# Kernel optimization log

Hardware: AMD Instinct MI355X
Metric: run time of the kernel (lower is better)

Reference implementation:

```python
import jax, jax.numpy as jnp
import numpy as np
from jax import lax

B, L = 1, 2048
D_MODEL = 768
D_INNER = 1536          # expand(2) * d_model
D_STATE = 16
DT_RANK = 48            # ceil(768/16)
D_CONV = 4
N_LAYER = 4
VOCAB = 50264           # 50257 padded to multiple of 8
EPS = 1e-5


def setup_inputs() -> dict:
    key = jax.random.key(0)
    ks = jax.random.split(key, 10)
    sc = 0.02
    input_ids = jax.random.randint(ks[0], (B, L), 0, VOCAB)
    emb = jax.random.normal(ks[1], (VOCAB, D_MODEL), jnp.float32) * sc
    in_proj_w = jax.random.normal(ks[2], (N_LAYER, 2 * D_INNER, D_MODEL), jnp.float32) * sc
    conv_w = jax.random.normal(ks[3], (N_LAYER, D_INNER, D_CONV), jnp.float32) * 0.1
    conv_b = jnp.zeros((N_LAYER, D_INNER), jnp.float32)
    x_proj_w = jax.random.normal(ks[4], (N_LAYER, DT_RANK + 2 * D_STATE, D_INNER), jnp.float32) * sc
    dt_proj_w = jax.random.normal(ks[5], (N_LAYER, D_INNER, DT_RANK), jnp.float32) * 0.1
    dt_proj_b = jax.random.normal(ks[6], (N_LAYER, D_INNER), jnp.float32) * 0.1
    # A_log initialized as log(1..d_state) repeated over d_inner (as in module init)
    A_row = jnp.log(jnp.arange(1, D_STATE + 1, dtype=jnp.float32))
    A_log = jnp.broadcast_to(A_row, (N_LAYER, D_INNER, D_STATE)).copy()
    D_param = jnp.ones((N_LAYER, D_INNER), jnp.float32)
    out_proj_w = jax.random.normal(ks[7], (N_LAYER, D_MODEL, D_INNER), jnp.float32) * sc
    norm_w = jnp.ones((N_LAYER, D_MODEL), jnp.float32)
    norm_f_w = jnp.ones((D_MODEL,), jnp.float32)
    return {
        'input_ids': input_ids, 'emb': emb, 'in_proj_w': in_proj_w,
        'conv_w': conv_w, 'conv_b': conv_b, 'x_proj_w': x_proj_w,
        'dt_proj_w': dt_proj_w, 'dt_proj_b': dt_proj_b, 'A_log': A_log,
        'D_param': D_param, 'out_proj_w': out_proj_w, 'norm_w': norm_w,
        'norm_f_w': norm_f_w,
    }


def _rmsnorm(x, w):
    return x * lax.rsqrt(jnp.mean(x * x, axis=-1, keepdims=True) + EPS) * w


def _selective_scan(u, delta, A, Bm, Cm, Dv):
    # u, delta: (b,l,d_in); A: (d_in,n); Bm, Cm: (b,l,n); Dv: (d_in,)
    deltaA = jnp.exp(delta[..., None] * A)                       # (b,l,d_in,n)
    deltaB_u = delta[..., None] * Bm[:, :, None, :] * u[..., None]  # (b,l,d_in,n)
    b = u.shape[0]
    h0 = jnp.zeros((b, D_INNER, D_STATE), u.dtype)

    def step(h, inp):
        dA_t, dBu_t, C_t = inp
        h = dA_t * h + dBu_t                                     # (b,d_in,n)
        y = jnp.einsum('bdn,bn->bd', h, C_t)
        return h, y

    xs = (jnp.swapaxes(deltaA, 0, 1), jnp.swapaxes(deltaB_u, 0, 1),
          jnp.swapaxes(Cm, 0, 1))
    _, ys = lax.scan(step, h0, xs)                               # (l,b,d_in)
    y = jnp.swapaxes(ys, 0, 1)
    return y + u * Dv


def _mamba_block(x, in_w, cw, cb, xp_w, dtp_w, dtp_b, A_log, Dv, out_w):
    b, l, _ = x.shape
    x_and_res = x @ in_w.T                                       # (b,l,2*d_in)
    xi, res = x_and_res[..., :D_INNER], x_and_res[..., D_INNER:]
    # depthwise causal conv1d
    xc = jnp.swapaxes(xi, 1, 2)                                  # (b,d_in,l)
    xc = lax.conv_general_dilated(
        xc, cw[:, None, :], window_strides=(1,), padding=[(D_CONV - 1, 0)],
        feature_group_count=D_INNER, dimension_numbers=('NCH', 'OIH', 'NCH'))
    xc = xc + cb[None, :, None]
    xi = jax.nn.silu(jnp.swapaxes(xc, 1, 2))                     # (b,l,d_in)
    # ssm
    A = -jnp.exp(A_log)
    x_dbl = xi @ xp_w.T                                          # (b,l,dt_rank+2n)
    delta = x_dbl[..., :DT_RANK]
    Bm = x_dbl[..., DT_RANK:DT_RANK + D_STATE]
    Cm = x_dbl[..., DT_RANK + D_STATE:]
    delta = jax.nn.softplus(delta @ dtp_w.T + dtp_b)             # (b,l,d_in)
    y = _selective_scan(xi, delta, A, Bm, Cm, Dv)
    y = y * jax.nn.silu(res)
    return y @ out_w.T


def reference(input_ids, emb, in_proj_w, conv_w, conv_b, x_proj_w,
              dt_proj_w, dt_proj_b, A_log, D_param, out_proj_w,
              norm_w, norm_f_w):
    x = emb[input_ids]                                           # (b,l,d_model)
    for i in range(N_LAYER):
        h = _rmsnorm(x, norm_w[i])
        x = x + _mamba_block(h, in_proj_w[i], conv_w[i], conv_b[i],
                             x_proj_w[i], dt_proj_w[i], dt_proj_b[i],
                             A_log[i], D_param[i], out_proj_w[i])
    x = _rmsnorm(x, norm_f_w)
    logits = x @ emb.T                                           # tied lm_head
    return logits
```

## Files before the change

### kernel.cpp

```cpp
#include <hip/hip_runtime.h>
#include <hip/hip_bf16.h>
#include <math.h>

#define LSEQ 2048
#define DMODEL 768
#define DINNER 1536
#define DSTATE 16
#define DTRANK 48
#define NLAYER 4
#define XDBL_W 80
#define CH 64
#define SLEN 32

typedef __attribute__((ext_vector_type(4))) float f32x4;
typedef __attribute__((ext_vector_type(8))) short short8;
typedef __attribute__((ext_vector_type(8))) __bf16 bf16x8;
typedef __attribute__((ext_vector_type(4))) unsigned short us4;

__device__ inline float softplus_f(float x) {
    return fmaxf(x, 0.f) + log1pf(expf(-fabsf(x)));
}
__device__ inline float silu_f(float x) {
    return x / (1.f + expf(-x));
}

__device__ inline unsigned short f2bf(float f) {
    unsigned int u = __float_as_uint(f);
    unsigned int r = (u + 0x7fffu + ((u >> 16) & 1u)) >> 16;
    return (unsigned short)r;
}
__device__ inline float bf2f(unsigned short b) {
    return __uint_as_float((unsigned int)b << 16);
}

__device__ inline f32x4 mfma_bf16_16x16x32(short8 a, short8 b, f32x4 c) {
    return __builtin_amdgcn_mfma_f32_16x16x32_bf16(
        __builtin_bit_cast(bf16x8, a), __builtin_bit_cast(bf16x8, b), c, 0, 0, 0);
}

#define GLDS16(gp, lp) __builtin_amdgcn_global_load_lds( \
    (const __attribute__((address_space(1))) void*)(gp), \
    (__attribute__((address_space(3))) void*)(lp), 16, 0, 0)

__global__ __launch_bounds__(256) void embed_kernel(
    const int* __restrict__ ids, const float* __restrict__ emb,
    float* __restrict__ x)
{
    int l = blockIdx.x;
    int id = ids[l];
    const float* src = emb + (size_t)id * DMODEL;
    float* dst = x + (size_t)l * DMODEL;
    for (int j = threadIdx.x; j < DMODEL; j += 256) dst[j] = src[j];
}

__global__ __launch_bounds__(256) void rmsnorm_kernel(
    const float* __restrict__ x, const float* __restrict__ w,
    float* __restrict__ o)
{
    int row = blockIdx.x;
    const float* xr = x + (size_t)row * DMODEL;
    float ss = 0.f;
    for (int j = threadIdx.x; j < DMODEL; j += 256) { float v = xr[j]; ss += v * v; }
    __shared__ float red[256];
    red[threadIdx.x] = ss;
    __syncthreads();
    for (int s = 128; s > 0; s >>= 1) {
        if (threadIdx.x < s) red[threadIdx.x] += red[threadIdx.x + s];
        __syncthreads();
    }
    float scale = rsqrtf(red[0] / DMODEL + 1e-5f);
    for (int j = threadIdx.x; j < DMODEL; j += 256)
        o[(size_t)row * DMODEL + j] = xr[j] * scale * w[j];
}

#define BM 64
#define BN 64
#define BK 16
__global__ __launch_bounds__(256) void gemm_nt(
    const float* __restrict__ A, const float* __restrict__ B,
    float* __restrict__ C, int M, int N, int K,
    int lda, int ldb, int ldc, int mode, const float* __restrict__ bias)
{
    __shared__ float As[BK][BM + 4];
    __shared__ float Bs[BK][BN + 4];
    int tid = threadIdx.x;
    int tx = tid & 15;
    int ty = tid >> 4;
    int row0 = blockIdx.y * BM;
    int col0 = blockIdx.x * BN;

    int lm = tid >> 2;
    int lk = (tid & 3) * 4;

    float acc[4][4];
#pragma unroll
    for (int i = 0; i < 4; ++i)
#pragma unroll
        for (int j = 0; j < 4; ++j) acc[i][j] = 0.f;

    for (int k0 = 0; k0 < K; k0 += BK) {
        {
            int gm = row0 + lm;
            float4 v = make_float4(0.f, 0.f, 0.f, 0.f);
            if (gm < M) v = *(const float4*)(A + (size_t)gm * lda + k0 + lk);
            As[lk + 0][lm] = v.x; As[lk + 1][lm] = v.y;
            As[lk + 2][lm] = v.z; As[lk + 3][lm] = v.w;
            int gn = col0 + lm;
            float4 w = make_float4(0.f, 0.f, 0.f, 0.f);
            if (gn < N) w = *(const float4*)(B + (size_t)gn * ldb + k0 + lk);
            Bs[lk + 0][lm] = w.x; Bs[lk + 1][lm] = w.y;
            Bs[lk + 2][lm] = w.z; Bs[lk + 3][lm] = w.w;
        }
        __syncthreads();
#pragma unroll
        for (int k = 0; k < BK; ++k) {
            float4 a = *(const float4*)(&As[k][ty * 4]);
            float4 b = *(const float4*)(&Bs[k][tx * 4]);
            float av[4] = { a.x, a.y, a.z, a.w };
            float bv[4] = { b.x, b.y, b.z, b.w };
#pragma unroll
            for (int i = 0; i < 4; ++i)
#pragma unroll
                for (int j = 0; j < 4; ++j) acc[i][j] += av[i] * bv[j];
        }
        __syncthreads();
    }

#pragma unroll
    for (int i = 0; i < 4; ++i) {
        int m = row0 + ty * 4 + i;
        if (m >= M) continue;
#pragma unroll
        for (int j = 0; j < 4; ++j) {
            int n = col0 + tx * 4 + j;
            if (n >= N) continue;
            float v = acc[i][j];
            if (mode == 1) v = softplus_f(v + bias[n]);
            else if (mode == 2) v += C[(size_t)m * ldc + n];
            C[(size_t)m * ldc + n] = v;
        }
    }
}

__global__ __launch_bounds__(256) void split_bf16_kernel(
    const float* __restrict__ src, unsigned short* __restrict__ hi,
    unsigned short* __restrict__ lo, long long srcElems, long long totElems)
{
    long long idx = ((long long)blockIdx.x * 256 + threadIdx.x) * 4;
    if (idx >= totElems) return;
    float4 v = make_float4(0.f, 0.f, 0.f, 0.f);
    if (idx < srcElems) v = *(const float4*)(src + idx);
    unsigned short h0 = f2bf(v.x), h1 = f2bf(v.y), h2 = f2bf(v.z), h3 = f2bf(v.w);
    us4 hv = { h0, h1, h2, h3 };
    us4 lv = { f2bf(v.x - bf2f(h0)), f2bf(v.y - bf2f(h1)),
               f2bf(v.z - bf2f(h2)), f2bf(v.w - bf2f(h3)) };
    *(us4*)(hi + idx) = hv;
    *(us4*)(lo + idx) = lv;
}

__global__ __launch_bounds__(256) void gemm_logits_mfma(
    const unsigned short* __restrict__ Ah, const unsigned short* __restrict__ Al,
    const unsigned short* __restrict__ Bh, const unsigned short* __restrict__ Bl,
    float* __restrict__ C, int N)
{
    __shared__ unsigned short As[128 * 32];
    __shared__ unsigned short Bs[128 * 32];
    int tid = threadIdx.x;
    int lane = tid & 63;
    int wid = tid >> 6;
    int wrow = wid >> 1, wcol = wid & 1;
    int brow0 = blockIdx.x * 128;
    int bcol0 = blockIdx.y * 128;

    f32x4 acc[4][4];
#pragma unroll
    for (int m = 0; m < 4; ++m)
#pragma unroll
        for (int n = 0; n < 4; ++n) acc[m][n] = (f32x4){ 0.f, 0.f, 0.f, 0.f };

    int arow = brow0 + wid * 32 + (lane >> 2);
    int bcol = bcol0 + wid * 32 + (lane >> 2);
    int kb = (lane & 3) * 8;
    char* lbaseA = (char*)As + wid * 2048;
    char* lbaseB = (char*)Bs + wid * 2048;

    for (int vb = 0; vb < 3; ++vb) {
        const unsigned short* Ab = (vb == 1) ? Al : Ah;
        const unsigned short* Bb = (vb == 2) ? Bl : Bh;
        for (int k0 = 0; k0 < DMODEL; k0 += 32) {
#pragma unroll
            for (int j = 0; j < 2; ++j) {
                GLDS16(Ab + (size_t)(arow + j * 16) * DMODEL + k0 + kb, lbaseA + j * 1024);
                GLDS16(Bb + (size_t)(bcol + j * 16) * DMODEL + k0 + kb, lbaseB + j * 1024);
            }
            __syncthreads();
            short8 af[4], bfr[4];
#pragma unroll
            for (int m = 0; m < 4; ++m)
                af[m] = *(const short8*)(As + ((wrow * 64 + m * 16 + (lane & 15)) * 32 + (lane >> 4) * 8));
#pragma unroll
            for (int n = 0; n < 4; ++n)
                bfr[n] = *(const short8*)(Bs + ((wcol * 64 + n * 16 + (lane & 15)) * 32 + (lane >> 4) * 8));
#pragma unroll
            for (int m = 0; m < 4; ++m)
#pragma unroll
                for (int n = 0; n < 4; ++n)
                    acc[m][n] = mfma_bf16_16x16x32(af[m], bfr[n], acc[m][n]);
            __syncthreads();
        }
    }

    int r0 = brow0 + wrow * 64 + (lane >> 4) * 4;
    int c0 = bcol0 + wcol * 64 + (lane & 15);
#pragma unroll
    for (int m = 0; m < 4; ++m)
#pragma unroll
        for (int n = 0; n < 4; ++n) {
            int col = c0 + n * 16;
            if (col >= N) continue;
#pragma unroll
            for (int i = 0; i < 4; ++i)
                C[(size_t)(r0 + m * 16 + i) * N + col] = acc[m][n][i];
        }
}

__global__ __launch_bounds__(256) void conv_silu_kernel(
    const float* __restrict__ xr, const float* __restrict__ cw,
    const float* __restrict__ cb, float* __restrict__ u)
{
    int idx = blockIdx.x * 256 + threadIdx.x;
    if (idx >= LSEQ * DINNER) return;
    int l = idx / DINNER;
    int d = idx - l * DINNER;
    float s = cb[d];
#pragma unroll
    for (int t = 0; t < 4; ++t) {
        int ll = l - 3 + t;
        if (ll >= 0) s += xr[(size_t)ll * (2 * DINNER) + d] * cw[d * 4 + t];
    }
    u[idx] = silu_f(s);
}

__global__ __launch_bounds__(256) void neg_exp_kernel(
    const float* __restrict__ a, float* __restrict__ o, int n)
{
    int i = blockIdx.x * 256 + threadIdx.x;
    if (i < n) o[i] = -expf(a[i]);
}

__global__ __launch_bounds__(256) void scan_phase1(
    const float* __restrict__ delta, const float* __restrict__ u,
    const float* __restrict__ xdbl, const float* __restrict__ Aneg,
    float* __restrict__ cA, float* __restrict__ cB)
{
    int tid = threadIdx.x;
    int n = tid & 15;
    int d = blockIdx.x * 16 + (tid >> 4);
    int c = blockIdx.y;
    float Av = Aneg[d * DSTATE + n];
    float h = 0.f, ap = 1.f;
    int l = c * SLEN;
    for (int s = 0; s < SLEN; ++s, ++l) {
        float dt = delta[(size_t)l * DINNER + d];
        float uv = u[(size_t)l * DINNER + d];
        float Bv = xdbl[l * XDBL_W + DTRANK + n];
        float a = expf(dt * Av);
        h = a * h + dt * Bv * uv;
        ap *= a;
    }
    size_t off = ((size_t)c * DINNER + d) * DSTATE + n;
    cA[off] = ap;
    cB[off] = h;
}

__global__ __launch_bounds__(256) void scan_phase2(
    const float* __restrict__ cA, const float* __restrict__ cB,
    float* __restrict__ hs)
{
    int idx = blockIdx.x * 256 + threadIdx.x;
    float h = 0.f;
    for (int c = 0; c < CH; ++c) {
        size_t off = (size_t)c * DINNER * DSTATE + idx;
        hs[off] = h;
        h = cA[off] * h + cB[off];
    }
}

__global__ __launch_bounds__(256) void scan_phase3(
    const float* __restrict__ delta, const float* __restrict__ u,
    const float* __restrict__ xdbl, const float* __restrict__ Aneg,
    const float* __restrict__ hs, const float* __restrict__ Dp,
    const float* __restrict__ xr, float* __restrict__ y)
{
    int tid = threadIdx.x;
    int n = tid & 15;
    int d = blockIdx.x * 16 + (tid >> 4);
    int c = blockIdx.y;
    float Av = Aneg[d * DSTATE + n];
    float Dv = Dp[d];
    float h = hs[((size_t)c * DINNER + d) * DSTATE + n];
    int l = c * SLEN;
    for (int s = 0; s < SLEN; ++s, ++l) {
        float dt = delta[(size_t)l * DINNER + d];
        float uv = u[(size_t)l * DINNER + d];
        float Bv = xdbl[l * XDBL_W + DTRANK + n];
        float Cv = xdbl[l * XDBL_W + DTRANK + DSTATE + n];
        float a = expf(dt * Av);
        h = a * h + dt * Bv * uv;
        float p = h * Cv;
        p += __shfl_down(p, 8, 16);
        p += __shfl_down(p, 4, 16);
        p += __shfl_down(p, 2, 16);
        p += __shfl_down(p, 1, 16);
        if (n == 0) {
            float r = xr[(size_t)l * (2 * DINNER) + DINNER + d];
            y[(size_t)l * DINNER + d] = (p + uv * Dv) * silu_f(r);
        }
    }
}

extern "C" void kernel_launch(void* const* d_in, const int* in_sizes, int n_in,
                              void* d_out, int out_size, void* d_ws, size_t ws_size,
                              hipStream_t stream)
{
    const int*   ids   = (const int*)d_in[0];
    const float* emb   = (const float*)d_in[1];
    const float* in_w  = (const float*)d_in[2];
    const float* cw    = (const float*)d_in[3];
    const float* cb    = (const float*)d_in[4];
    const float* xpw   = (const float*)d_in[5];
    const float* dtw   = (const float*)d_in[6];
    const float* dtb   = (const float*)d_in[7];
    const float* A_log = (const float*)d_in[8];
    const float* Dp    = (const float*)d_in[9];
    const float* ow    = (const float*)d_in[10];
    const float* nw    = (const float*)d_in[11];
    const float* nfw   = (const float*)d_in[12];
    float* out = (float*)d_out;

    const int VOCAB = in_sizes[1] / DMODEL;
    const int Npad = ((VOCAB + 127) / 128) * 128;

    float* ws = (float*)d_ws;
    size_t o = 0;
    float* x     = ws + o; o += (size_t)LSEQ * DMODEL;
    float* h     = ws + o; o += (size_t)LSEQ * DMODEL;
    float* xr    = ws + o; o += (size_t)LSEQ * 2 * DINNER;
    float* u     = ws + o; o += (size_t)LSEQ * DINNER;
    float* xdbl  = ws + o; o += (size_t)LSEQ * XDBL_W;
    float* delta = ws + o; o += (size_t)LSEQ * DINNER;
    float* Aneg  = ws + o; o += (size_t)DINNER * DSTATE;
    float* cA    = ws + o; o += (size_t)CH * DINNER * DSTATE;
    float* cB    = ws + o; o += (size_t)CH * DINNER * DSTATE;
    float* hsb   = ws + o; o += (size_t)CH * DINNER * DSTATE;
    float* y     = ws + o; o += (size_t)LSEQ * DINNER;
    unsigned short* Ahi = (unsigned short*)(ws + o); o += (size_t)LSEQ * DMODEL / 2;
    unsigned short* Alo = (unsigned short*)(ws + o); o += (size_t)LSEQ * DMODEL / 2;
    unsigned short* Bhi = (unsigned short*)(ws + o); o += (size_t)Npad * DMODEL / 2;
    unsigned short* Blo = (unsigned short*)(ws + o); o += (size_t)Npad * DMODEL / 2;

    {
        long long srcElems = (long long)VOCAB * DMODEL;
        long long totElems = (long long)Npad * DMODEL;
        int nb = (int)((totElems / 4 + 255) / 256);
        split_bf16_kernel<<<nb, 256, 0, stream>>>(emb, Bhi, Blo, srcElems, totElems);
    }

    embed_kernel<<<LSEQ, 256, 0, stream>>>(ids, emb, x);

    for (int i = 0; i < NLAYER; ++i) {
        rmsnorm_kernel<<<LSEQ, 256, 0, stream>>>(x, nw + (size_t)i * DMODEL, h);

        gemm_nt<<<dim3(2 * DINNER / BN, LSEQ / BM), 256, 0, stream>>>(
            h, in_w + (size_t)i * 2 * DINNER * DMODEL, xr,
            LSEQ, 2 * DINNER, DMODEL, DMODEL, DMODEL, 2 * DINNER, 0, nullptr);

        conv_silu_kernel<<<(LSEQ * DINNER + 255) / 256, 256, 0, stream>>>(
            xr, cw + (size_t)i * DINNER * 4, cb + (size_t)i * DINNER, u);

        gemm_nt<<<dim3((XDBL_W + BN - 1) / BN, LSEQ / BM), 256, 0, stream>>>(
            u, xpw + (size_t)i * XDBL_W * DINNER, xdbl,
            LSEQ, XDBL_W, DINNER, DINNER, DINNER, XDBL_W, 0, nullptr);

        gemm_nt<<<dim3(DINNER / BN, LSEQ / BM), 256, 0, stream>>>(
            xdbl, dtw + (size_t)i * DINNER * DTRANK, delta,
            LSEQ, DINNER, DTRANK, XDBL_W, DTRANK, DINNER, 1,
            dtb + (size_t)i * DINNER);

        neg_exp_kernel<<<(DINNER * DSTATE + 255) / 256, 256, 0, stream>>>(
            A_log + (size_t)i * DINNER * DSTATE, Aneg, DINNER * DSTATE);

        scan_phase1<<<dim3(DINNER / 16, CH), 256, 0, stream>>>(
            delta, u, xdbl, Aneg, cA, cB);
        scan_phase2<<<DINNER * DSTATE / 256, 256, 0, stream>>>(cA, cB, hsb);
        scan_phase3<<<dim3(DINNER / 16, CH), 256, 0, stream>>>(
            delta, u, xdbl, Aneg, hsb, Dp + (size_t)i * DINNER, xr, y);

        gemm_nt<<<dim3(DMODEL / BN, LSEQ / BM), 256, 0, stream>>>(
            y, ow + (size_t)i * DMODEL * DINNER, x,
            LSEQ, DMODEL, DINNER, DINNER, DINNER, DMODEL, 2, nullptr);
    }

    rmsnorm_kernel<<<LSEQ, 256, 0, stream>>>(x, nfw, h);

    {
        long long aElems = (long long)LSEQ * DMODEL;
        int nb = (int)((aElems / 4 + 255) / 256);
        split_bf16_kernel<<<nb, 256, 0, stream>>>(h, Ahi, Alo, aElems, aElems);
    }

    gemm_logits_mfma<<<dim3(LSEQ / 128, Npad / 128), 256, 0, stream>>>(
        Ahi, Alo, Bhi, Blo, out, VOCAB);
}
```

Measured before the change: 3.350 ms.

## Move all layer GEMMs to split-bf16 MFMA with swizzled LDS and fused producers

Replaces the scalar FP32 tiled GEMM for the in_proj, x_proj, dt_proj and out_proj matmuls with a generalized 3-pass hi/lo bf16 MFMA GEMM. Producer kernels (rmsnorm, conv_silu, scan_phase3) now emit hi/lo bf16 splits directly. The dt_proj is folded into a precomputed combined weight (dt_w @ x_proj_w[:48]) so delta comes straight from u via one large GEMM. It also adds an XOR swizzle on LDS to avoid bank conflicts, a grouped block-index remap for L2 locality, and a single hoisted neg_exp for all layers. The cost is extra per-call weight-split kernels and a larger K=1536 delta GEMM in place of the rank-48 one, which also changes the rounding path slightly.

```diff
diff --git a/kernel.cpp b/kernel.cpp
--- a/kernel.cpp
+++ b/kernel.cpp
@@ -53,9 +53,9 @@
     for (int j = threadIdx.x; j < DMODEL; j += 256) dst[j] = src[j];
 }
 
-__global__ __launch_bounds__(256) void rmsnorm_kernel(
+__global__ __launch_bounds__(256) void rmsnorm_split_kernel(
     const float* __restrict__ x, const float* __restrict__ w,
-    float* __restrict__ o)
+    unsigned short* __restrict__ ohi, unsigned short* __restrict__ olo)
 {
     int row = blockIdx.x;
     const float* xr = x + (size_t)row * DMODEL;
@@ -69,76 +69,11 @@
         __syncthreads();
     }
     float scale = rsqrtf(red[0] / DMODEL + 1e-5f);
-    for (int j = threadIdx.x; j < DMODEL; j += 256)
-        o[(size_t)row * DMODEL + j] = xr[j] * scale * w[j];
-}
-
-#define BM 64
-#define BN 64
-#define BK 16
-__global__ __launch_bounds__(256) void gemm_nt(
-    const float* __restrict__ A, const float* __restrict__ B,
-    float* __restrict__ C, int M, int N, int K,
-    int lda, int ldb, int ldc, int mode, const float* __restrict__ bias)
-{
-    __shared__ float As[BK][BM + 4];
-    __shared__ float Bs[BK][BN + 4];
-    int tid = threadIdx.x;
-    int tx = tid & 15;
-    int ty = tid >> 4;
-    int row0 = blockIdx.y * BM;
-    int col0 = blockIdx.x * BN;
-
-    int lm = tid >> 2;
-    int lk = (tid & 3) * 4;
-
-    float acc[4][4];
-#pragma unroll
-    for (int i = 0; i < 4; ++i)
-#pragma unroll
-        for (int j = 0; j < 4; ++j) acc[i][j] = 0.f;
-
-    for (int k0 = 0; k0 < K; k0 += BK) {
-        {
-            int gm = row0 + lm;
-            float4 v = make_float4(0.f, 0.f, 0.f, 0.f);
-            if (gm < M) v = *(const float4*)(A + (size_t)gm * lda + k0 + lk);
-            As[lk + 0][lm] = v.x; As[lk + 1][lm] = v.y;
-            As[lk + 2][lm] = v.z; As[lk + 3][lm] = v.w;
-            int gn = col0 + lm;
-            float4 w = make_float4(0.f, 0.f, 0.f, 0.f);
-            if (gn < N) w = *(const float4*)(B + (size_t)gn * ldb + k0 + lk);
-            Bs[lk + 0][lm] = w.x; Bs[lk + 1][lm] = w.y;
-            Bs[lk + 2][lm] = w.z; Bs[lk + 3][lm] = w.w;
-        }
-        __syncthreads();
-#pragma unroll
-        for (int k = 0; k < BK; ++k) {
-            float4 a = *(const float4*)(&As[k][ty * 4]);
-            float4 b = *(const float4*)(&Bs[k][tx * 4]);
-            float av[4] = { a.x, a.y, a.z, a.w };
-            float bv[4] = { b.x, b.y, b.z, b.w };
-#pragma unroll
-            for (int i = 0; i < 4; ++i)
-#pragma unroll
-                for (int j = 0; j < 4; ++j) acc[i][j] += av[i] * bv[j];
-        }
-        __syncthreads();
-    }
-
-#pragma unroll
-    for (int i = 0; i < 4; ++i) {
-        int m = row0 + ty * 4 + i;
-        if (m >= M) continue;
-#pragma unroll
-        for (int j = 0; j < 4; ++j) {
-            int n = col0 + tx * 4 + j;
-            if (n >= N) continue;
-            float v = acc[i][j];
-            if (mode == 1) v = softplus_f(v + bias[n]);
-            else if (mode == 2) v += C[(size_t)m * ldc + n];
-            C[(size_t)m * ldc + n] = v;
-        }
+    for (int j = threadIdx.x; j < DMODEL; j += 256) {
+        float v = xr[j] * scale * w[j];
+        unsigned short hv = f2bf(v);
+        ohi[(size_t)row * DMODEL + j] = hv;
+        olo[(size_t)row * DMODEL + j] = f2bf(v - bf2f(hv));
     }
 }
 
@@ -158,10 +93,52 @@
     *(us4*)(lo + idx) = lv;
 }
 
-__global__ __launch_bounds__(256) void gemm_logits_mfma(
+__global__ __launch_bounds__(256) void wdelta_kernel(
+    const float* __restrict__ dtw, const float* __restrict__ xpw,
+    unsigned short* __restrict__ whi, unsigned short* __restrict__ wlo)
+{
+    __shared__ float As[64][49];
+    __shared__ float Bs[48][65];
+    int tid = threadIdx.x;
+    int tx = tid & 15, ty = tid >> 4;
+    int i0 = blockIdx.y * 64, j0 = blockIdx.x * 64;
+    for (int t = tid; t < 64 * 48; t += 256)
+        As[t / 48][t % 48] = dtw[(size_t)(i0 + t / 48) * DTRANK + (t % 48)];
+    for (int t = tid; t < 48 * 64; t += 256)
+        Bs[t / 64][t % 64] = xpw[(size_t)(t / 64) * DINNER + j0 + (t % 64)];
+    __syncthreads();
+    float acc[4][4];
+#pragma unroll
+    for (int i = 0; i < 4; ++i)
+#pragma unroll
+        for (int j = 0; j < 4; ++j) acc[i][j] = 0.f;
+    for (int k = 0; k < 48; ++k) {
+        float a[4], b[4];
+#pragma unroll
+        for (int i = 0; i < 4; ++i) a[i] = As[ty * 4 + i][k];
+#pragma unroll
+        for (int j = 0; j < 4; ++j) b[j] = Bs[k][tx * 4 + j];
+#pragma unroll
+        for (int i = 0; i < 4; ++i)
+#pragma unroll
+            for (int j = 0; j < 4; ++j) acc[i][j] += a[i] * b[j];
+    }
+#pragma unroll
+    for (int i = 0; i < 4; ++i)
+#pragma unroll
+        for (int j = 0; j < 4; ++j) {
+            size_t off = (size_t)(i0 + ty * 4 + i) * DINNER + j0 + tx * 4 + j;
+            unsigned short h = f2bf(acc[i][j]);
+            whi[off] = h;
+            wlo[off] = f2bf(acc[i][j] - bf2f(h));
+        }
+}
+
+__global__ __launch_bounds__(256) void gemm_mfma_split(
     const unsigned short* __restrict__ Ah, const unsigned short* __restrict__ Al,
     const unsigned short* __restrict__ Bh, const unsigned short* __restrict__ Bl,
-    float* __restrict__ C, int N)
+    float* __restrict__ C, int mtiles, int Nreal, int K, int ldc, int mode,
+    const float* __restrict__ bias)
 {
     __shared__ unsigned short As[128 * 32];
     __shared__ unsigned short Bs[128 * 32];
@@ -169,8 +146,11 @@
     int lane = tid & 63;
     int wid = tid >> 6;
     int wrow = wid >> 1, wcol = wid & 1;
-    int brow0 = blockIdx.x * 128;
-    int bcol0 = blockIdx.y * 128;
+
+    int chunk = gridDim.x >> 3;
+    int wg = (blockIdx.x & 7) * chunk + (blockIdx.x >> 3);
+    int brow0 = (wg % mtiles) * 128;
+    int bcol0 = (wg / mtiles) * 128;
 
     f32x4 acc[4][4];
 #pragma unroll
@@ -178,29 +158,33 @@
 #pragma unroll
         for (int n = 0; n < 4; ++n) acc[m][n] = (f32x4){ 0.f, 0.f, 0.f, 0.f };
 
-    int arow = brow0 + wid * 32 + (lane >> 2);
-    int bcol = bcol0 + wid * 32 + (lane >> 2);
-    int kb = (lane & 3) * 8;
+    int rl0 = wid * 32 + (lane >> 2);
     char* lbaseA = (char*)As + wid * 2048;
     char* lbaseB = (char*)Bs + wid * 2048;
 
     for (int vb = 0; vb < 3; ++vb) {
         const unsigned short* Ab = (vb == 1) ? Al : Ah;
         const unsigned short* Bb = (vb == 2) ? Bl : Bh;
-        for (int k0 = 0; k0 < DMODEL; k0 += 32) {
+        for (int k0 = 0; k0 < K; k0 += 32) {
 #pragma unroll
             for (int j = 0; j < 2; ++j) {
-                GLDS16(Ab + (size_t)(arow + j * 16) * DMODEL + k0 + kb, lbaseA + j * 1024);
-                GLDS16(Bb + (size_t)(bcol + j * 16) * DMODEL + k0 + kb, lbaseB + j * 1024);
+                int rl = rl0 + j * 16;
+                int cg = ((lane & 3) ^ ((rl >> 1) & 3)) * 8;
+                GLDS16(Ab + (size_t)(brow0 + rl) * K + k0 + cg, lbaseA + j * 1024);
+                GLDS16(Bb + (size_t)(bcol0 + rl) * K + k0 + cg, lbaseB + j * 1024);
             }
             __syncthreads();
             short8 af[4], bfr[4];
 #pragma unroll
-            for (int m = 0; m < 4; ++m)
-                af[m] = *(const short8*)(As + ((wrow * 64 + m * 16 + (lane & 15)) * 32 + (lane >> 4) * 8));
-#pragma unroll
-            for (int n = 0; n < 4; ++n)
-                bfr[n] = *(const short8*)(Bs + ((wcol * 64 + n * 16 + (lane & 15)) * 32 + (lane >> 4) * 8));
+            for (int m = 0; m < 4; ++m) {
+                int r = wrow * 64 + m * 16 + (lane & 15);
+                af[m] = *(const short8*)(As + r * 32 + (((lane >> 4) ^ ((r >> 1) & 3)) * 8));
+            }
+#pragma unroll
+            for (int n = 0; n < 4; ++n) {
+                int r = wcol * 64 + n * 16 + (lane & 15);
+                bfr[n] = *(const short8*)(Bs + r * 32 + (((lane >> 4) ^ ((r >> 1) & 3)) * 8));
+            }
 #pragma unroll
             for (int m = 0; m < 4; ++m)
 #pragma unroll
@@ -217,16 +201,22 @@
 #pragma unroll
         for (int n = 0; n < 4; ++n) {
             int col = c0 + n * 16;
-            if (col >= N) continue;
-#pragma unroll
-            for (int i = 0; i < 4; ++i)
-                C[(size_t)(r0 + m * 16 + i) * N + col] = acc[m][n][i];
+            if (col >= Nreal) continue;
+#pragma unroll
+            for (int i = 0; i < 4; ++i) {
+                int row = r0 + m * 16 + i;
+                float v = acc[m][n][i];
+                if (mode == 1) v = softplus_f(v + bias[col]);
+                else if (mode == 2) v += C[(size_t)row * ldc + col];
+                C[(size_t)row * ldc + col] = v;
+            }
         }
 }
 
 __global__ __launch_bounds__(256) void conv_silu_kernel(
     const float* __restrict__ xr, const float* __restrict__ cw,
-    const float* __restrict__ cb, float* __restrict__ u)
+    const float* __restrict__ cb, float* __restrict__ u,
+    unsigned short* __restrict__ uhi, unsigned short* __restrict__ ulo)
 {
     int idx = blockIdx.x * 256 + threadIdx.x;
     if (idx >= LSEQ * DINNER) return;
@@ -238,7 +228,11 @@
         int ll = l - 3 + t;
         if (ll >= 0) s += xr[(size_t)ll * (2 * DINNER) + d] * cw[d * 4 + t];
     }
-    u[idx] = silu_f(s);
+    float v = silu_f(s);
+    u[idx] = v;
+    unsigned short h = f2bf(v);
+    uhi[idx] = h;
+    ulo[idx] = f2bf(v - bf2f(h));
 }
 
 __global__ __launch_bounds__(256) void neg_exp_kernel(
@@ -290,7 +284,8 @@
     const float* __restrict__ delta, const float* __restrict__ u,
     const float* __restrict__ xdbl, const float* __restrict__ Aneg,
     const float* __restrict__ hs, const float* __restrict__ Dp,
-    const float* __restrict__ xr, float* __restrict__ y)
+    const float* __restrict__ xr,
+    unsigned short* __restrict__ yhi, unsigned short* __restrict__ ylo)
 {
     int tid = threadIdx.x;
     int n = tid & 15;
@@ -314,7 +309,11 @@
         p += __shfl_down(p, 1, 16);
         if (n == 0) {
             float r = xr[(size_t)l * (2 * DINNER) + DINNER + d];
-            y[(size_t)l * DINNER + d] = (p + uv * Dv) * silu_f(r);
+            float vy = (p + uv * Dv) * silu_f(r);
+            size_t oy = (size_t)l * DINNER + d;
+            unsigned short hv = f2bf(vy);
+            yhi[oy] = hv;
+            ylo[oy] = f2bf(vy - bf2f(hv));
         }
     }
 }
@@ -344,71 +343,92 @@
     float* ws = (float*)d_ws;
     size_t o = 0;
     float* x     = ws + o; o += (size_t)LSEQ * DMODEL;
-    float* h     = ws + o; o += (size_t)LSEQ * DMODEL;
     float* xr    = ws + o; o += (size_t)LSEQ * 2 * DINNER;
     float* u     = ws + o; o += (size_t)LSEQ * DINNER;
     float* xdbl  = ws + o; o += (size_t)LSEQ * XDBL_W;
     float* delta = ws + o; o += (size_t)LSEQ * DINNER;
-    float* Aneg  = ws + o; o += (size_t)DINNER * DSTATE;
+    float* Aneg  = ws + o; o += (size_t)NLAYER * DINNER * DSTATE;
     float* cA    = ws + o; o += (size_t)CH * DINNER * DSTATE;
     float* cB    = ws + o; o += (size_t)CH * DINNER * DSTATE;
     float* hsb   = ws + o; o += (size_t)CH * DINNER * DSTATE;
-    float* y     = ws + o; o += (size_t)LSEQ * DINNER;
-    unsigned short* Ahi = (unsigned short*)(ws + o); o += (size_t)LSEQ * DMODEL / 2;
-    unsigned short* Alo = (unsigned short*)(ws + o); o += (size_t)LSEQ * DMODEL / 2;
+    unsigned short* hhi = (unsigned short*)(ws + o); o += (size_t)LSEQ * DMODEL / 2;
+    unsigned short* hlo = (unsigned short*)(ws + o); o += (size_t)LSEQ * DMODEL / 2;
+    unsigned short* uhi = (unsigned short*)(ws + o); o += (size_t)LSEQ * DINNER / 2;
+    unsigned short* ulo = (unsigned short*)(ws + o); o += (size_t)LSEQ * DINNER / 2;
+    unsigned short* yhi = (unsigned short*)(ws + o); o += (size_t)LSEQ * DINNER / 2;
+    unsigned short* ylo = (unsigned short*)(ws + o); o += (size_t)LSEQ * DINNER / 2;
     unsigned short* Bhi = (unsigned short*)(ws + o); o += (size_t)Npad * DMODEL / 2;
     unsigned short* Blo = (unsigned short*)(ws + o); o += (size_t)Npad * DMODEL / 2;
+    unsigned short* wAh = (unsigned short*)(ws + o); o += (size_t)2 * DINNER * DMODEL / 2;
+    unsigned short* wAl = (unsigned short*)(ws + o); o += (size_t)2 * DINNER * DMODEL / 2;
+    unsigned short* wOh = (unsigned short*)(ws + o); o += (size_t)DMODEL * DINNER / 2;
+    unsigned short* wOl = (unsigned short*)(ws + o); o += (size_t)DMODEL * DINNER / 2;
+    unsigned short* wXh = (unsigned short*)(ws + o); o += (size_t)128 * DINNER / 2;
+    unsigned short* wXl = (unsigned short*)(ws + o); o += (size_t)128 * DINNER / 2;
+    unsigned short* wDh = (unsigned short*)(ws + o); o += (size_t)DINNER * DINNER / 2;
+    unsigned short* wDl = (unsigned short*)(ws + o); o += (size_t)DINNER * DINNER / 2;
 
     {
-        long long srcElems = (long long)VOCAB * DMODEL;
-        long long totElems = (long long)Npad * DMODEL;
-        int nb = (int)((totElems / 4 + 255) / 256);
-        split_bf16_kernel<<<nb, 256, 0, stream>>>(emb, Bhi, Blo, srcElems, totElems);
-    }
+        long long srcE = (long long)VOCAB * DMODEL;
+        long long totE = (long long)Npad * DMODEL;
+        split_bf16_kernel<<<(int)((totE / 4 + 255) / 256), 256, 0, stream>>>(
+            emb, Bhi, Blo, srcE, totE);
+    }
+    neg_exp_kernel<<<(NLAYER * DINNER * DSTATE + 255) / 256, 256, 0, stream>>>(
+        A_log, Aneg, NLAYER * DINNER * DSTATE);
 
     embed_kernel<<<LSEQ, 256, 0, stream>>>(ids, emb, x);
 
     for (int i = 0; i < NLAYER; ++i) {
-        rmsnorm_kernel<<<LSEQ, 256, 0, stream>>>(x, nw + (size_t)i * DMODEL, h);
-
-        gemm_nt<<<dim3(2 * DINNER / BN, LSEQ / BM), 256, 0, stream>>>(
-            h, in_w + (size_t)i * 2 * DINNER * DMODEL, xr,
-            LSEQ, 2 * DINNER, DMODEL, DMODEL, DMODEL, 2 * DINNER, 0, nullptr);
+        {
+            long long e = (long long)2 * DINNER * DMODEL;
+            split_bf16_kernel<<<(int)((e / 4 + 255) / 256), 256, 0, stream>>>(
+                in_w + (size_t)i * e, wAh, wAl, e, e);
+        }
+        {
+            long long e = (long long)DMODEL * DINNER;
+            split_bf16_kernel<<<(int)((e / 4 + 255) / 256), 256, 0, stream>>>(
+                ow + (size_t)i * e, wOh, wOl, e, e);
+        }
+        {
+            long long srcE = (long long)XDBL_W * DINNER;
+            long long totE = (long long)128 * DINNER;
+            split_bf16_kernel<<<(int)((totE / 4 + 255) / 256), 256, 0, stream>>>(
+                xpw + (size_t)i * srcE, wXh, wXl, srcE, totE);
+        }
+        wdelta_kernel<<<dim3(DINNER / 64, DINNER / 64), 256, 0, stream>>>(
+            dtw + (size_t)i * DINNER * DTRANK, xpw + (size_t)i * XDBL_W * DINNER,
+            wDh, wDl);
+
+        rmsnorm_split_kernel<<<LSEQ, 256, 0, stream>>>(
+            x, nw + (size_t)i * DMODEL, hhi, hlo);
+
+        gemm_mfma_split<<<16 * (2 * DINNER / 128), 256, 0, stream>>>(
+            hhi, hlo, wAh, wAl, xr, 16, 2 * DINNER, DMODEL, 2 * DINNER, 0, nullptr);
 
         conv_silu_kernel<<<(LSEQ * DINNER + 255) / 256, 256, 0, stream>>>(
-            xr, cw + (size_t)i * DINNER * 4, cb + (size_t)i * DINNER, u);
-
-        gemm_nt<<<dim3((XDBL_W + BN - 1) / BN, LSEQ / BM), 256, 0, stream>>>(
-            u, xpw + (size_t)i * XDBL_W * DINNER, xdbl,
-            LSEQ, XDBL_W, DINNER, DINNER, DINNER, XDBL_W, 0, nullptr);
-
-        gemm_nt<<<dim3(DINNER / BN, LSEQ / BM), 256, 0, stream>>>(
-            xdbl, dtw + (size_t)i * DINNER * DTRANK, delta,
-            LSEQ, DINNER, DTRANK, XDBL_W, DTRANK, DINNER, 1,
+            xr, cw + (size_t)i * DINNER * 4, cb + (size_t)i * DINNER, u, uhi, ulo);
+
+        gemm_mfma_split<<<16 * 1, 256, 0, stream>>>(
+            uhi, ulo, wXh, wXl, xdbl, 16, XDBL_W, DINNER, XDBL_W, 0, nullptr);
+
+        gemm_mfma_split<<<16 * (DINNER / 128), 256, 0, stream>>>(
+            uhi, ulo, wDh, wDl, delta, 16, DINNER, DINNER, DINNER, 1,
             dtb + (size_t)i * DINNER);
 
-        neg_exp_kernel<<<(DINNER * DSTATE + 255) / 256, 256, 0, stream>>>(
-            A_log + (size_t)i * DINNER * DSTATE, Aneg, DINNER * DSTATE);
-
         scan_phase1<<<dim3(DINNER / 16, CH), 256, 0, stream>>>(
-            delta, u, xdbl, Aneg, cA, cB);
+            delta, u, xdbl, Aneg + (size_t)i * DINNER * DSTATE, cA, cB);
         scan_phase2<<<DINNER * DSTATE / 256, 256, 0, stream>>>(cA, cB, hsb);
         scan_phase3<<<dim3(DINNER / 16, CH), 256, 0, stream>>>(
-            delta, u, xdbl, Aneg, hsb, Dp + (size_t)i * DINNER, xr, y);
-
-        gemm_nt<<<dim3(DMODEL / BN, LSEQ / BM), 256, 0, stream>>>(
-            y, ow + (size_t)i * DMODEL * DINNER, x,
-            LSEQ, DMODEL, DINNER, DINNER, DINNER, DMODEL, 2, nullptr);
-    }
-
-    rmsnorm_kernel<<<LSEQ, 256, 0, stream>>>(x, nfw, h);
-
-    {
-        long long aElems = (long long)LSEQ * DMODEL;
-        int nb = (int)((aElems / 4 + 255) / 256);
-        split_bf16_kernel<<<nb, 256, 0, stream>>>(h, Ahi, Alo, aElems, aElems);
-    }
-
-    gemm_logits_mfma<<<dim3(LSEQ / 128, Npad / 128), 256, 0, stream>>>(
-        Ahi, Alo, Bhi, Blo, out, VOCAB);
-}
+            delta, u, xdbl, Aneg + (size_t)i * DINNER * DSTATE, hsb,
+            Dp + (size_t)i * DINNER, xr, yhi, ylo);
+
+        gemm_mfma_split<<<16 * (DMODEL / 128), 256, 0, stream>>>(
+            yhi, ylo, wOh, wOl, x, 16, DMODEL, DINNER, DMODEL, 2, nullptr);
+    }
+
+    rmsnorm_split_kernel<<<LSEQ, 256, 0, stream>>>(x, nfw, hhi, hlo);
+
+    gemm_mfma_split<<<16 * (Npad / 128), 256, 0, stream>>>(
+        hhi, hlo, Bhi, Blo, out, 16, VOCAB, DMODEL, VOCAB, 0, nullptr);
+}
```

After: 3.412 ms. About the same (+1.8%).
